# Performance work log

Measured on AMD Instinct MI355X. Metric: run time of the kernel, lower is better.

Reference implementation:

```python
import jax, jax.numpy as jnp
import numpy as np

N_NODES = 50000
N_EDGES = 800000
N_GRAPHS = 1024
IN_DIM, HID, OUT_DIM = 78, 256, 128
EPS = 1e-5


def setup_inputs() -> dict:
    key = jax.random.key(0)
    ks = jax.random.split(key, 12)
    def lin(k, fi, fo):
        s = 1.0 / np.sqrt(fi)
        return jax.random.uniform(k, (fi, fo), jnp.float32, -s, s)
    inp = {
        "x_l": jax.random.normal(ks[0], (N_NODES, IN_DIM), jnp.float32),
        "edge_index_l": jax.random.randint(ks[1], (2, N_EDGES), 0, N_NODES, jnp.int64),
        "batch_l": jnp.sort(jax.random.randint(ks[2], (N_NODES,), 0, N_GRAPHS, jnp.int64)),
        # GraphConv 1: 78 -> 256 (lin_rel has bias, lin_root no bias)
        "W1_rel": lin(ks[3], IN_DIM, HID), "b1_rel": jnp.zeros((HID,), jnp.float32), "W1_root": lin(ks[4], IN_DIM, HID),
        # GraphConv 2: 256 -> 512
        "W2_rel": lin(ks[5], HID, 2 * HID), "b2_rel": jnp.zeros((2 * HID,), jnp.float32), "W2_root": lin(ks[6], HID, 2 * HID),
        # GraphConv 3: 512 -> 512
        "W3_rel": lin(ks[7], 2 * HID, 2 * HID), "b3_rel": jnp.zeros((2 * HID,), jnp.float32), "W3_root": lin(ks[8], 2 * HID, 2 * HID),
        # fc1: Linear(512 -> 128) + LayerNorm(128); Dropout(0.01) is identity in eval
        "W_fc": lin(ks[9], 2 * HID, OUT_DIM), "b_fc": jnp.zeros((OUT_DIM,), jnp.float32),
        "ln_g": jnp.ones((OUT_DIM,), jnp.float32), "ln_b": jnp.zeros((OUT_DIM,), jnp.float32),
    }
    return inp


def _graph_conv(x, src, dst, W_rel, b_rel, W_root):
    # PyG GraphConv (aggr='add'): out = lin_rel(sum_{j->i} x_j) + lin_root(x_i)
    aggr = jax.ops.segment_sum(x[src], dst, num_segments=x.shape[0])  # [N, d_in]
    return aggr @ W_rel + b_rel + x @ W_root


def reference(x_l, edge_index_l, batch_l,
              W1_rel, b1_rel, W1_root,
              W2_rel, b2_rel, W2_root,
              W3_rel, b3_rel, W3_root,
              W_fc, b_fc, ln_g, ln_b):
    src, dst = edge_index_l[0], edge_index_l[1]
    h = jax.nn.relu(_graph_conv(x_l, src, dst, W1_rel, b1_rel, W1_root))
    h = jax.nn.relu(_graph_conv(h, src, dst, W2_rel, b2_rel, W2_root))
    h = jax.nn.relu(_graph_conv(h, src, dst, W3_rel, b3_rel, W3_root))
    # fc1: Linear -> LayerNorm -> Dropout(0.01, identity in eval) -> ReLU
    z = h @ W_fc + b_fc
    mu = jnp.mean(z, axis=-1, keepdims=True)
    var = jnp.mean(jnp.square(z - mu), axis=-1, keepdims=True)
    z = (z - mu) * jax.lax.rsqrt(var + EPS) * ln_g + ln_b
    x_atom = jax.nn.relu(z)  # [N, OUT_DIM]
    pooled = jax.ops.segment_sum(x_atom, batch_l, num_segments=N_GRAPHS)  # [G, OUT_DIM]
    return (x_atom, pooled)
```

## Files before the change

### kernel.cpp

```cpp
#include <hip/hip_runtime.h>

#define N_NODES 50000
#define N_EDGES 800000
#define N_GRAPHS 1024
#define IN_DIM 78
#define K1P 96
#define HID 256
#define OUT_DIM 128

typedef unsigned short ushort_t;
typedef __attribute__((ext_vector_type(8))) short v8s;
typedef __attribute__((ext_vector_type(4))) float v4f;
typedef __attribute__((ext_vector_type(4))) unsigned int u4;
typedef __attribute__((ext_vector_type(2))) unsigned short us2;
typedef __attribute__((ext_vector_type(4))) unsigned short us4;
typedef __attribute__((ext_vector_type(8))) unsigned short us8;

__device__ __forceinline__ ushort_t f2bf(float f) {
    unsigned u = __float_as_uint(f);
    unsigned r = (u + 0x7fffu + ((u >> 16) & 1u)) >> 16;
    return (ushort_t)r;
}
__device__ __forceinline__ float bf2f(ushort_t h) {
    return __uint_as_float((unsigned)h << 16);
}

__global__ __launch_bounds__(256)
void wt_all_kernel(const float* __restrict__ W1r, const float* __restrict__ W1o,
                   const float* __restrict__ W2r, const float* __restrict__ W2o,
                   const float* __restrict__ W3r, const float* __restrict__ W3o,
                   const float* __restrict__ Wfc, ushort_t* __restrict__ out)
{
    int i = blockIdx.x * 256 + threadIdx.x;
    if (i >= 901120) return;
    const float* W; int K, N, Kp, base;
    if      (i < 24576)  { W = W1r; K = IN_DIM; N = HID;     Kp = 96;  base = 0; }
    else if (i < 49152)  { W = W1o; K = IN_DIM; N = HID;     Kp = 96;  base = 24576; }
    else if (i < 180224) { W = W2r; K = HID;    N = 2 * HID; Kp = 256; base = 49152; }
    else if (i < 311296) { W = W2o; K = HID;    N = 2 * HID; Kp = 256; base = 180224; }
    else if (i < 573440) { W = W3r; K = 2*HID;  N = 2 * HID; Kp = 512; base = 311296; }
    else if (i < 835584) { W = W3o; K = 2*HID;  N = 2 * HID; Kp = 512; base = 573440; }
    else                 { W = Wfc; K = 2*HID;  N = OUT_DIM; Kp = 512; base = 835584; }
    int j = i - base;
    int n = j / Kp, k = j - n * Kp;
    float v = (k < K) ? W[(size_t)k * N + n] : 0.0f;
    out[i] = f2bf(v);
}

__global__ __launch_bounds__(256)
void pad_cast_kernel(const float* __restrict__ in, ushort_t* __restrict__ out,
                     int rows, int Kin, int Kout)
{
    int i = blockIdx.x * 256 + threadIdx.x;
    if (i >= rows * Kout) return;
    int r = i / Kout, k = i - r * Kout;
    out[i] = f2bf(k < Kin ? in[(size_t)r * Kin + k] : 0.0f);
}

__global__ __launch_bounds__(256)
void hist_kernel(const int* __restrict__ dstI, int* __restrict__ deg, int nE)
{
    int e = blockIdx.x * 256 + threadIdx.x;
    if (e < nE) {
        int d = dstI[e];
        if ((unsigned)d < (unsigned)N_NODES) atomicAdd(&deg[d], 1);
    }
}

__global__ __launch_bounds__(1024)
void scan1_kernel(const int* __restrict__ deg, int* __restrict__ rowptr,
                  int* __restrict__ blocksum, int n)
{
    __shared__ int s[1024];
    int b = (int)blockIdx.x, t = (int)threadIdx.x;
    int i = b * 1024 + t;
    int v = (i < n) ? deg[i] : 0;
    s[t] = v;
    __syncthreads();
    for (int off = 1; off < 1024; off <<= 1) {
        int a = (t >= off) ? s[t - off] : 0;
        __syncthreads();
        s[t] += a;
        __syncthreads();
    }
    if (i < n) rowptr[i + 1] = s[t];
    if (t == 1023) blocksum[b] = s[1023];
    if (b == 0 && t == 0) rowptr[0] = 0;
}

__global__ __launch_bounds__(64)
void scan2_kernel(int* __restrict__ blocksum, int nb)
{
    int t = (int)threadIdx.x;
    int v = (t < nb) ? blocksum[t] : 0;
    #pragma unroll
    for (int off = 1; off < 64; off <<= 1) {
        int a = __shfl_up(v, off, 64);
        if (t >= off) v += a;
    }
    if (t < nb) blocksum[t] = v;
}

__global__ __launch_bounds__(256)
void scan3_kernel(const int* __restrict__ blocksum, int* __restrict__ rowptr,
                  int* __restrict__ cursor, int n)
{
    int j = blockIdx.x * 256 + threadIdx.x;
    if (j > n) return;
    int v;
    if (j == 0) v = 0;
    else {
        int b = (j - 1) >> 10;
        v = rowptr[j] + (b >= 1 ? blocksum[b - 1] : 0);
    }
    rowptr[j] = v;
    if (j < n) cursor[j] = v;
}

__global__ __launch_bounds__(256)
void fill_kernel(const int* __restrict__ srcI, const int* __restrict__ dstI,
                 int* __restrict__ cursor, int* __restrict__ csr_src, int nE)
{
    int e = blockIdx.x * 256 + threadIdx.x;
    if (e < nE) {
        int d = dstI[e];
        int s = srcI[e];
        if ((unsigned)d < (unsigned)N_NODES && (unsigned)s < (unsigned)N_NODES) {
            int pos = atomicAdd(&cursor[d], 1);
            csr_src[pos] = s;
        }
    }
}

template<int VPT> struct VecT;
template<> struct VecT<2> { using T = us2; };
template<> struct VecT<4> { using T = us4; };
template<> struct VecT<8> { using T = us8; };

template<int VPT>
__global__ __launch_bounds__(256)
void csr_agg_wave_kernel(const ushort_t* __restrict__ feat,
                         const int* __restrict__ rowptr,
                         const int* __restrict__ csr_src,
                         ushort_t* __restrict__ out, int Ds)
{
    using T = typename VecT<VPT>::T;
    const int wv   = (int)threadIdx.x >> 6;
    const int node = (int)blockIdx.x * 4 + wv;
    if (node >= N_NODES) return;
    const int lane = (int)threadIdx.x & 63;
    const int off0 = lane * VPT;
    const bool act = off0 < Ds;
    const int off  = act ? off0 : (Ds - VPT);

    const int e0 = rowptr[node], e1 = rowptr[node + 1];
    float acc[VPT];
    #pragma unroll
    for (int i = 0; i < VPT; ++i) acc[i] = 0.0f;

    int e = e0;
    for (; e + 8 <= e1; e += 8) {
        T r[8];
        #pragma unroll
        for (int u = 0; u < 8; ++u) {
            int s = csr_src[e + u];
            r[u] = *(const T*)(feat + (size_t)s * Ds + off);
        }
        #pragma unroll
        for (int u = 0; u < 8; ++u)
            #pragma unroll
            for (int i = 0; i < VPT; ++i) acc[i] += bf2f(r[u][i]);
    }
    for (; e + 4 <= e1; e += 4) {
        T r[4];
        #pragma unroll
        for (int u = 0; u < 4; ++u) {
            int s = csr_src[e + u];
            r[u] = *(const T*)(feat + (size_t)s * Ds + off);
        }
        #pragma unroll
        for (int u = 0; u < 4; ++u)
            #pragma unroll
            for (int i = 0; i < VPT; ++i) acc[i] += bf2f(r[u][i]);
    }
    for (; e < e1; ++e) {
        int s = csr_src[e];
        T r = *(const T*)(feat + (size_t)s * Ds + off);
        #pragma unroll
        for (int i = 0; i < VPT; ++i) acc[i] += bf2f(r[i]);
    }

    if (act) {
        T o;
        #pragma unroll
        for (int i = 0; i < VPT; ++i) o[i] = f2bf(acc[i]);
        *(T*)(out + (size_t)node * Ds + off0) = o;
    }
}

template<int NT>
__global__ __launch_bounds__(256, 2)
void mfma_gemm_kernel(const ushort_t* __restrict__ A1,
                      const ushort_t* __restrict__ A2,
                      const ushort_t* __restrict__ W1t,
                      const ushort_t* __restrict__ W2t,
                      const float* __restrict__ bias,
                      void* __restrict__ outp,
                      int M, int K, int Fo, int relu, int out_bf16)
{
    constexpr int BN    = NT * 32;
    constexpr int NBT   = NT * 2;
    constexpr int BT_PW = NBT / 4;
    __shared__ __align__(16) ushort_t Al[8 * 512];
    __shared__ __align__(16) ushort_t Bl[NBT * 512];
    const int tid = (int)threadIdx.x;
    const int l   = tid & 63;
    const int w   = tid >> 6;
    const int q   = l >> 4;
    const int r15 = l & 15;
    const int bm  = blockIdx.y * 128;
    const int bn  = blockIdx.x * BN;
    const int wm  = w >> 1, wn = w & 1;

    const int s1 = K >> 5;
    const int nsteps = A2 ? (2 * s1) : s1;

    v4f acc[4][NT];
    #pragma unroll
    for (int mt = 0; mt < 4; ++mt)
        #pragma unroll
        for (int nt = 0; nt < NT; ++nt)
            acc[mt][nt] = (v4f){0.0f, 0.0f, 0.0f, 0.0f};

    u4 ra[2], rb[BT_PW];
    auto load_step = [&](int step) {
        const ushort_t* A  = (step >= s1) ? A2  : A1;
        const ushort_t* Bt = (step >= s1) ? W2t : W1t;
        const int k0 = ((step >= s1) ? (step - s1) : step) << 5;
        #pragma unroll
        for (int ii = 0; ii < 2; ++ii) {
            int it  = w * 2 + ii;
            int row = bm + it * 16 + r15;
            if (row < M) ra[ii] = *(const u4*)(A + (size_t)row * K + k0 + q * 8);
            else         ra[ii] = (u4){0u, 0u, 0u, 0u};
        }
        #pragma unroll
        for (int jj = 0; jj < BT_PW; ++jj) {
            int jt  = w * BT_PW + jj;
            int col = bn + jt * 16 + r15;
            rb[jj] = *(const u4*)(Bt + (size_t)col * K + k0 + q * 8);
        }
    };

    load_step(0);
    for (int step = 0; step < nsteps; ++step) {
        __syncthreads();
        #pragma unroll
        for (int ii = 0; ii < 2; ++ii)
            *(u4*)(Al + (size_t)(w * 2 + ii) * 512 + l * 8) = ra[ii];
        #pragma unroll
        for (int jj = 0; jj < BT_PW; ++jj)
            *(u4*)(Bl + (size_t)(w * BT_PW + jj) * 512 + l * 8) = rb[jj];
        if (step + 1 < nsteps) load_step(step + 1);
        __syncthreads();
        v8s af[4], bf[NT];
        #pragma unroll
        for (int mt = 0; mt < 4; ++mt)
            af[mt] = *(const v8s*)(Al + (size_t)(wm * 4 + mt) * 512 + l * 8);
        #pragma unroll
        for (int nt = 0; nt < NT; ++nt)
            bf[nt] = *(const v8s*)(Bl + (size_t)(wn * NT + nt) * 512 + l * 8);
        #pragma unroll
        for (int mt = 0; mt < 4; ++mt)
            #pragma unroll
            for (int nt = 0; nt < NT; ++nt)
                acc[mt][nt] = __builtin_amdgcn_mfma_f32_16x16x32_bf16(
                    af[mt], bf[nt], acc[mt][nt], 0, 0, 0);
    }

    #pragma unroll
    for (int nt = 0; nt < NT; ++nt) {
        int col = bn + wn * (NT * 16) + nt * 16 + r15;
        float bb = bias[col];
        #pragma unroll
        for (int mt = 0; mt < 4; ++mt) {
            #pragma unroll
            for (int p = 0; p < 4; ++p) {
                int row = bm + wm * 64 + mt * 16 + q * 4 + p;
                if (row < M) {
                    float v = acc[mt][nt][p] + bb;
                    if (relu) v = fmaxf(v, 0.0f);
                    if (out_bf16) ((ushort_t*)outp)[(size_t)row * Fo + col] = f2bf(v);
                    else          ((float*)outp)[(size_t)row * Fo + col]   = v;
                }
            }
        }
    }
}

__global__ __launch_bounds__(128)
void ln_relu_pool_kernel(const float* __restrict__ z,
                         const float* __restrict__ gamma,
                         const float* __restrict__ beta,
                         const int* __restrict__ batch,
                         float* __restrict__ x_atom,
                         float* __restrict__ pooled)
{
    int row = (int)blockIdx.x;
    int t = (int)threadIdx.x;
    float v = z[(long long)row * 128 + t];

    __shared__ float red[2];
    float s = v;
    #pragma unroll
    for (int o = 32; o >= 1; o >>= 1) s += __shfl_xor(s, o, 64);
    int wave = t >> 6;
    if ((t & 63) == 0) red[wave] = s;
    __syncthreads();
    float mean = (red[0] + red[1]) * (1.0f / 128.0f);

    float d = v - mean;
    float s2 = d * d;
    #pragma unroll
    for (int o = 32; o >= 1; o >>= 1) s2 += __shfl_xor(s2, o, 64);
    __syncthreads();
    if ((t & 63) == 0) red[wave] = s2;
    __syncthreads();
    float var = (red[0] + red[1]) * (1.0f / 128.0f);

    float y = d * rsqrtf(var + 1e-5f) * gamma[t] + beta[t];
    y = fmaxf(y, 0.0f);
    x_atom[(long long)row * 128 + t] = y;
    int b = batch[row];
    if ((unsigned)b < (unsigned)N_GRAPHS)
        atomicAdd(pooled + (long long)b * 128 + t, y);
}

extern "C" void kernel_launch(void* const* d_in, const int* in_sizes, int n_in,
                              void* d_out, int out_size, void* d_ws, size_t ws_size,
                              hipStream_t stream)
{
    const float* x     = (const float*)d_in[0];
    const int*   ei    = (const int*)d_in[1];
    const int*   batch = (const int*)d_in[2];
    const float* W1r   = (const float*)d_in[3];
    const float* b1    = (const float*)d_in[4];
    const float* W1o   = (const float*)d_in[5];
    const float* W2r   = (const float*)d_in[6];
    const float* b2    = (const float*)d_in[7];
    const float* W2o   = (const float*)d_in[8];
    const float* W3r   = (const float*)d_in[9];
    const float* b3    = (const float*)d_in[10];
    const float* W3o   = (const float*)d_in[11];
    const float* Wfc   = (const float*)d_in[12];
    const float* bfc   = (const float*)d_in[13];
    const float* lng   = (const float*)d_in[14];
    const float* lnb   = (const float*)d_in[15];

    const size_t WS_NEED = 204800000;
    if (ws_size < WS_NEED) {
        hipMemsetAsync(d_out, 0, (size_t)out_size * sizeof(float), stream);
        return;
    }

    char* ws = (char*)d_ws;
    ushort_t* xb   = (ushort_t*)(ws + 0);
    ushort_t* h1   = (ushort_t*)(ws + 9600000);
    float*    z    = (float*)   (ws + 0);
    ushort_t* aggr = (ushort_t*)(ws + 35200000);
    ushort_t* h2   = (ushort_t*)(ws + 86400000);
    ushort_t* h3   = (ushort_t*)(ws + 137600000);
    int* deg    = (int*)(ws + 188800000);
    int* rowptr = (int*)(ws + 189000000);
    int* cursor = (int*)(ws + 189200128);
    int* csrsrc = (int*)(ws + 189400128);
    int* blksum = (int*)(ws + 192600128);
    ushort_t* wt = (ushort_t*)(ws + 192600512);
    ushort_t* w1r_t = wt;
    ushort_t* w1o_t = wt + 24576;
    ushort_t* w2r_t = wt + 49152;
    ushort_t* w2o_t = wt + 180224;
    ushort_t* w3r_t = wt + 311296;
    ushort_t* w3o_t = wt + 573440;
    ushort_t* wfc_t = wt + 835584;

    float* x_atom = (float*)d_out;
    float* pooled = x_atom + (size_t)N_NODES * OUT_DIM;

    const int* src = ei;
    const int* dst = ei + N_EDGES;

    wt_all_kernel<<<(901120 + 255) / 256, 256, 0, stream>>>(W1r, W1o, W2r, W2o,
                                                            W3r, W3o, Wfc, wt);
    pad_cast_kernel<<<((N_NODES * K1P) + 255) / 256, 256, 0, stream>>>(x, xb, N_NODES, IN_DIM, K1P);

    hipMemsetAsync(deg, 0, N_NODES * sizeof(int), stream);
    hist_kernel<<<(N_EDGES + 255) / 256, 256, 0, stream>>>(dst, deg, N_EDGES);
    {
        int nb = (N_NODES + 1023) / 1024;
        scan1_kernel<<<nb, 1024, 0, stream>>>(deg, rowptr, blksum, N_NODES);
        scan2_kernel<<<1, 64, 0, stream>>>(blksum, nb);
        scan3_kernel<<<(N_NODES + 1 + 255) / 256, 256, 0, stream>>>(blksum, rowptr, cursor, N_NODES);
    }
    fill_kernel<<<(N_EDGES + 255) / 256, 256, 0, stream>>>(src, dst, cursor, csrsrc, N_EDGES);

    const int GY = (N_NODES + 127) / 128;
    const int AGG_BLKS = (N_NODES + 3) / 4;

    csr_agg_wave_kernel<2><<<AGG_BLKS, 256, 0, stream>>>(xb, rowptr, csrsrc, aggr, K1P);
    {
        dim3 g(HID / 256, GY);
        mfma_gemm_kernel<8><<<g, 256, 0, stream>>>(aggr, xb, w1r_t, w1o_t, b1, h1,
                                                   N_NODES, K1P, HID, 1, 1);
    }
    csr_agg_wave_kernel<4><<<AGG_BLKS, 256, 0, stream>>>(h1, rowptr, csrsrc, aggr, HID);
    {
        dim3 g((2 * HID) / 256, GY);
        mfma_gemm_kernel<8><<<g, 256, 0, stream>>>(aggr, h1, w2r_t, w2o_t, b2, h2,
                                                   N_NODES, HID, 2 * HID, 1, 1);
    }
    csr_agg_wave_kernel<8><<<AGG_BLKS, 256, 0, stream>>>(h2, rowptr, csrsrc, aggr, 2 * HID);
    {
        dim3 g((2 * HID) / 256, GY);
        mfma_gemm_kernel<8><<<g, 256, 0, stream>>>(aggr, h2, w3r_t, w3o_t, b3, h3,
                                                   N_NODES, 2 * HID, 2 * HID, 1, 1);
    }
    {
        dim3 g(OUT_DIM / 128, GY);
        mfma_gemm_kernel<4><<<g, 256, 0, stream>>>(h3, nullptr, wfc_t, nullptr, bfc, z,
                                                   N_NODES, 2 * HID, OUT_DIM, 0, 0);
    }
    hipMemsetAsync(pooled, 0, (size_t)N_GRAPHS * OUT_DIM * sizeof(float), stream);
    ln_relu_pool_kernel<<<N_NODES, 128, 0, stream>>>(z, lng, lnb, batch, x_atom, pooled);
}
```

Baseline: 692.7 us.

## Fuse fc1 GEMM with LayerNorm, ReLU and graph pooling in one kernel

Replaces the separate fc1 MFMA GEMM and the per-row LayerNorm/pool kernel with a single kernel. Each block computes a 128x128 tile of z, stages it in shared memory, computes per-row mean and rstd, then writes x_atom and atomically accumulates into pooled. This removes the fp32 z round trip through global memory and one launch. In exchange the LN statistics loop is serial over 128 threads, and the new GEMM uses its own simpler double-buffered pipeline.

```diff
diff --git a/kernel.cpp b/kernel.cpp
--- a/kernel.cpp
+++ b/kernel.cpp
@@ -298,42 +298,124 @@
     }
 }
 
-__global__ __launch_bounds__(128)
-void ln_relu_pool_kernel(const float* __restrict__ z,
-                         const float* __restrict__ gamma,
-                         const float* __restrict__ beta,
-                         const int* __restrict__ batch,
-                         float* __restrict__ x_atom,
-                         float* __restrict__ pooled)
-{
-    int row = (int)blockIdx.x;
-    int t = (int)threadIdx.x;
-    float v = z[(long long)row * 128 + t];
-
-    __shared__ float red[2];
-    float s = v;
+__global__ __launch_bounds__(256, 2)
+void fc_ln_pool_kernel(const ushort_t* __restrict__ A,
+                       const ushort_t* __restrict__ Bt,
+                       const float* __restrict__ bias,
+                       const float* __restrict__ gamma,
+                       const float* __restrict__ beta,
+                       const int* __restrict__ batch,
+                       float* __restrict__ x_atom,
+                       float* __restrict__ pooled)
+{
+    constexpr int K = 512;
+    constexpr int ZS = 133;
+    __shared__ __align__(16) char smem[128 * ZS * 4 + 2 * 128 * 4];
+    ushort_t* Al = (ushort_t*)smem;
+    ushort_t* Bl = (ushort_t*)(smem + 8192);
+    float*    zt = (float*)smem;
+    float*  mu_s = (float*)(smem + 128 * ZS * 4);
+    float*  rs_s = mu_s + 128;
+
+    const int tid = (int)threadIdx.x;
+    const int l   = tid & 63;
+    const int w   = tid >> 6;
+    const int q   = l >> 4;
+    const int r15 = l & 15;
+    const int bm  = blockIdx.x * 128;
+    const int wm  = w >> 1, wn = w & 1;
+
+    const int nsteps = K >> 5;
+
+    v4f acc[4][4];
     #pragma unroll
-    for (int o = 32; o >= 1; o >>= 1) s += __shfl_xor(s, o, 64);
-    int wave = t >> 6;
-    if ((t & 63) == 0) red[wave] = s;
+    for (int mt = 0; mt < 4; ++mt)
+        #pragma unroll
+        for (int nt = 0; nt < 4; ++nt)
+            acc[mt][nt] = (v4f){0.0f, 0.0f, 0.0f, 0.0f};
+
+    u4 ra[2], rb[2];
+    auto load_step = [&](int step) {
+        const int k0 = step << 5;
+        #pragma unroll
+        for (int ii = 0; ii < 2; ++ii) {
+            int it  = w * 2 + ii;
+            int row = bm + it * 16 + r15;
+            if (row < N_NODES) ra[ii] = *(const u4*)(A + (size_t)row * K + k0 + q * 8);
+            else               ra[ii] = (u4){0u, 0u, 0u, 0u};
+        }
+        #pragma unroll
+        for (int jj = 0; jj < 2; ++jj) {
+            int jt  = w * 2 + jj;
+            int col = jt * 16 + r15;
+            rb[jj] = *(const u4*)(Bt + (size_t)col * K + k0 + q * 8);
+        }
+    };
+
+    load_step(0);
+    for (int step = 0; step < nsteps; ++step) {
+        __syncthreads();
+        #pragma unroll
+        for (int ii = 0; ii < 2; ++ii)
+            *(u4*)(Al + (size_t)(w * 2 + ii) * 512 + l * 8) = ra[ii];
+        #pragma unroll
+        for (int jj = 0; jj < 2; ++jj)
+            *(u4*)(Bl + (size_t)(w * 2 + jj) * 512 + l * 8) = rb[jj];
+        if (step + 1 < nsteps) load_step(step + 1);
+        __syncthreads();
+        v8s af[4], bf[4];
+        #pragma unroll
+        for (int mt = 0; mt < 4; ++mt)
+            af[mt] = *(const v8s*)(Al + (size_t)(wm * 4 + mt) * 512 + l * 8);
+        #pragma unroll
+        for (int nt = 0; nt < 4; ++nt)
+            bf[nt] = *(const v8s*)(Bl + (size_t)(wn * 4 + nt) * 512 + l * 8);
+        #pragma unroll
+        for (int mt = 0; mt < 4; ++mt)
+            #pragma unroll
+            for (int nt = 0; nt < 4; ++nt)
+                acc[mt][nt] = __builtin_amdgcn_mfma_f32_16x16x32_bf16(
+                    af[mt], bf[nt], acc[mt][nt], 0, 0, 0);
+    }
+
     __syncthreads();
-    float mean = (red[0] + red[1]) * (1.0f / 128.0f);
-
-    float d = v - mean;
-    float s2 = d * d;
     #pragma unroll
-    for (int o = 32; o >= 1; o >>= 1) s2 += __shfl_xor(s2, o, 64);
+    for (int nt = 0; nt < 4; ++nt) {
+        int col = wn * 64 + nt * 16 + r15;
+        float bb = bias[col];
+        #pragma unroll
+        for (int mt = 0; mt < 4; ++mt) {
+            #pragma unroll
+            for (int p = 0; p < 4; ++p) {
+                int rr = wm * 64 + mt * 16 + q * 4 + p;
+                zt[rr * ZS + col] = acc[mt][nt][p] + bb;
+            }
+        }
+    }
     __syncthreads();
-    if ((t & 63) == 0) red[wave] = s2;
+    if (tid < 128) {
+        const float* zr = zt + tid * ZS;
+        float s = 0.0f;
+        for (int j = 0; j < 128; ++j) s += zr[j];
+        float m = s * (1.0f / 128.0f);
+        float v = 0.0f;
+        for (int j = 0; j < 128; ++j) { float d = zr[j] - m; v += d * d; }
+        mu_s[tid] = m;
+        rs_s[tid] = rsqrtf(v * (1.0f / 128.0f) + 1e-5f);
+    }
     __syncthreads();
-    float var = (red[0] + red[1]) * (1.0f / 128.0f);
-
-    float y = d * rsqrtf(var + 1e-5f) * gamma[t] + beta[t];
-    y = fmaxf(y, 0.0f);
-    x_atom[(long long)row * 128 + t] = y;
-    int b = batch[row];
-    if ((unsigned)b < (unsigned)N_GRAPHS)
-        atomicAdd(pooled + (long long)b * 128 + t, y);
+    for (int i = tid; i < 128 * 128; i += 256) {
+        int r = i >> 7, c = i & 127;
+        int row = bm + r;
+        if (row < N_NODES) {
+            float y = (zt[r * ZS + c] - mu_s[r]) * rs_s[r] * gamma[c] + beta[c];
+            y = fmaxf(y, 0.0f);
+            x_atom[(size_t)row * 128 + c] = y;
+            int b = batch[row];
+            if ((unsigned)b < (unsigned)N_GRAPHS)
+                atomicAdd(pooled + (size_t)b * 128 + c, y);
+        }
+    }
 }
 
 extern "C" void kernel_launch(void* const* d_in, const int* in_sizes, int n_in,
@@ -366,7 +448,6 @@
     char* ws = (char*)d_ws;
     ushort_t* xb   = (ushort_t*)(ws + 0);
     ushort_t* h1   = (ushort_t*)(ws + 9600000);
-    float*    z    = (float*)   (ws + 0);
     ushort_t* aggr = (ushort_t*)(ws + 35200000);
     ushort_t* h2   = (ushort_t*)(ws + 86400000);
     ushort_t* h3   = (ushort_t*)(ws + 137600000);
@@ -425,11 +506,7 @@
         mfma_gemm_kernel<8><<<g, 256, 0, stream>>>(aggr, h2, w3r_t, w3o_t, b3, h3,
                                                    N_NODES, 2 * HID, 2 * HID, 1, 1);
     }
-    {
-        dim3 g(OUT_DIM / 128, GY);
-        mfma_gemm_kernel<4><<<g, 256, 0, stream>>>(h3, nullptr, wfc_t, nullptr, bfc, z,
-                                                   N_NODES, 2 * HID, OUT_DIM, 0, 0);
-    }
     hipMemsetAsync(pooled, 0, (size_t)N_GRAPHS * OUT_DIM * sizeof(float), stream);
-    ln_relu_pool_kernel<<<N_NODES, 128, 0, stream>>>(z, lng, lnb, batch, x_atom, pooled);
-}
+    fc_ln_pool_kernel<<<GY, 256, 0, stream>>>(h3, wfc_t, bfc, lng, lnb, batch,
+                                              x_atom, pooled);
+}
```

Result: no change. 699.1 us (+0.9%).
